# Performance work log

Measured on AMD Instinct MI355X. Metric: run time of the kernel, lower is better.

## Reference

```python
import jax, jax.numpy as jnp
import numpy as np

CODEBOOK_SIZE = 1024
CODEBOOK_DIM = 256
B, H, W = 32, 64, 64


def setup_inputs() -> dict:
    key = jax.random.key(0)
    kx, kc = jax.random.split(key)
    x = jax.random.normal(kx, (B, CODEBOOK_DIM, H, W), dtype=jnp.float32)
    # nn.init.uniform_(weight, -1/K, 1/K)
    bound = 1.0 / CODEBOOK_SIZE
    codebook = jax.random.uniform(kc, (CODEBOOK_SIZE, CODEBOOK_DIM),
                                  minval=-bound, maxval=bound, dtype=jnp.float32)
    return {"x": x, "codebook": codebook}


def reference(x, codebook):
    b, c, h, w = x.shape
    z_e = jnp.transpose(x, (0, 2, 3, 1))            # [b,h,w,c]
    z_flat = z_e.reshape(-1, c)                      # [N,c]
    # squared L2 distances: ||z||^2 + ||e||^2 - 2 z.e
    dists = (jnp.sum(z_flat * z_flat, axis=1, keepdims=True)
             + jnp.sum(codebook * codebook, axis=1)
             - 2.0 * jnp.matmul(z_flat, codebook.T))  # [N,K]
    idx = jnp.argmin(dists, axis=1)                  # [N] int
    z_q = codebook[idx].reshape(b, h, w, c)          # [b,h,w,c]
    # commitment + codebook loss (both detach patterns)
    loss = (jnp.mean((jax.lax.stop_gradient(z_e) - z_q) ** 2)
            + jnp.mean((jax.lax.stop_gradient(z_q) - z_e) ** 2))
    # straight-through estimator
    z_q_st = z_e + jax.lax.stop_gradient(z_q - z_e)
    z_q_out = jnp.transpose(z_q_st, (0, 3, 1, 2))    # [b,c,h,w]
    return z_q_out, idx, loss
```

## Files before the change

kernel.cpp:

```cpp
#include <hip/hip_runtime.h>


typedef __attribute__((ext_vector_type(8))) short short8;
typedef __attribute__((ext_vector_type(4))) float f32x4;
typedef unsigned long long u64;

#define IDX_OFF   33554432u
#define LOSS_OFF  33685504u
#define IMG_BYTE  67108864u
#define CAND_BYTE 68157440u
#define ENRM_BYTE 69206016u

__device__ __forceinline__ unsigned short f2bf(float f) {
  unsigned u = __float_as_uint(f);
  unsigned r = (u + 0x7FFFu + ((u >> 16) & 1u)) >> 16;
  return (unsigned short)r;
}

#define COMB(r) __fadd_rn(__fadd_rn(__fadd_rn(r[0], r[1]), __fadd_rn(r[2], r[3])), \
                          __fadd_rn(__fadd_rn(r[4], r[5]), __fadd_rn(r[6], r[7])))

extern "C" __global__ __launch_bounds__(256) void vq_r10_k0(const float* __restrict__ cb,
                                                            unsigned char* __restrict__ img,
                                                            float* __restrict__ outf) {
  unsigned tid = blockIdx.x * 256u + threadIdx.x;
  unsigned code = tid >> 7, dp = tid & 127u;
  const float* p = cb + (size_t)code * 256u + dp * 2u;
  unsigned u = ((unsigned)f2bf(p[1]) << 16) | (unsigned)f2bf(p[0]);
  unsigned kc = code >> 6, n = (code >> 4) & 3, c16 = code & 15;
  unsigned ks = dp >> 4, g = (dp >> 2) & 3, j = dp & 3;
  unsigned byte = kc * 32768u + (n * 8u + ks) * 1024u + (g * 16u + c16) * 16u + j * 4u;
  *(unsigned*)(img + byte) = u;
  if (tid == 0) outf[LOSS_OFF] = 0.0f;
}

extern "C" __global__ __launch_bounds__(256) void vq_r10_k0b(const float* __restrict__ cb,
                                                             float* __restrict__ enrm) {
#pragma clang fp contract(off)
  int c = blockIdx.x * 256 + threadIdx.x;
  const float* e = cb + (size_t)c * 256u;
  float h[2];
#pragma unroll
  for (int half = 0; half < 2; ++half) {
    float r[8];
#pragma unroll
    for (int j = 0; j < 8; ++j) {
      float v = e[half * 128 + j];
      r[j] = __fmul_rn(v, v);
    }
    for (int i = 8; i < 128; i += 8) {
#pragma unroll
      for (int j = 0; j < 8; ++j) {
        float v = e[half * 128 + i + j];
        r[j] = __fadd_rn(r[j], __fmul_rn(v, v));
      }
    }
    h[half] = COMB(r);
  }
  enrm[c] = __fadd_rn(h[0], h[1]);
}

extern "C" __global__ __launch_bounds__(256, 2) void vq_r10_k1(const float* __restrict__ x,
                                                               const unsigned char* __restrict__ img,
                                                               u64* __restrict__ cand4) {
  __shared__ __attribute__((aligned(16))) char lds[32768];
  const int t = threadIdx.x;
  const int bid = blockIdx.x;
  const int lane = t & 63;
  const int w = t >> 6;
  const int g = lane >> 4, c16 = lane & 15;

  const size_t xbase = (size_t)(bid >> 4) * 1048576u + (size_t)(bid & 15) * 256u;

  short8 a[4][8];
  for (int q = 0; q < 4; ++q) {
#pragma unroll 4
    for (int s = 0; s < 8; ++s) {
      int flat = s * 256 + t;
      int pt4 = flat & 15;
      int dp = flat >> 4;
      const float* px = x + xbase + (size_t)(2 * dp) * 4096u + (unsigned)(q * 64 + pt4 * 4);
      float4 fa = *(const float4*)px;
      float4 fb = *(const float4*)(px + 4096);
      const float* fap = (const float*)&fa;
      const float* fbp = (const float*)&fb;
#pragma unroll
      for (int k = 0; k < 4; ++k) {
        unsigned u = ((unsigned)f2bf(fbp[k]) << 16) | (unsigned)f2bf(fap[k]);
        int r = pt4 * 4 + k;
        *(unsigned*)(lds + r * 512 + ((dp * 4) ^ ((r & 31) << 2))) = u;
      }
    }
    __syncthreads();
    if (w == q) {
#pragma unroll
      for (int m = 0; m < 4; ++m) {
        const int r = m * 16 + c16;
        const int rsw = (r & 31) << 2;
#pragma unroll
        for (int ks = 0; ks < 8; ++ks) {
          union { unsigned q4[4]; short8 s8; } uu;
#pragma unroll
          for (int jj = 0; jj < 4; ++jj)
            uu.q4[jj] = *(const unsigned*)(lds + r * 512 + (((ks * 16 + g * 4 + jj) * 4) ^ rsw));
          a[m][ks] = uu.s8;
        }
      }
    }
    __syncthreads();
  }

  float t1[16], t2[16];
#pragma unroll
  for (int s = 0; s < 16; ++s) { t1[s] = -__builtin_inff(); t2[s] = -__builtin_inff(); }

  const unsigned char* bp = img + (unsigned)(lane * 16);
  for (int kc = 0; kc < 16; ++kc) {
    const unsigned char* bkc = bp + (unsigned)(kc * 32768);
#pragma unroll
    for (int n = 0; n < 4; ++n) {
      short8 bf[8];
#pragma unroll
      for (int ks = 0; ks < 8; ++ks)
        bf[ks] = *(const short8*)(bkc + (unsigned)((n * 8 + ks) * 1024));
      f32x4 acc0 = (f32x4){0.f, 0.f, 0.f, 0.f};
      f32x4 acc1 = (f32x4){0.f, 0.f, 0.f, 0.f};
      f32x4 acc2 = (f32x4){0.f, 0.f, 0.f, 0.f};
      f32x4 acc3 = (f32x4){0.f, 0.f, 0.f, 0.f};
#pragma unroll
      for (int ks = 0; ks < 8; ++ks) {
        acc0 = __builtin_amdgcn_mfma_f32_16x16x32_bf16(a[0][ks], bf[ks], acc0, 0, 0, 0);
        acc1 = __builtin_amdgcn_mfma_f32_16x16x32_bf16(a[1][ks], bf[ks], acc1, 0, 0, 0);
        acc2 = __builtin_amdgcn_mfma_f32_16x16x32_bf16(a[2][ks], bf[ks], acc2, 0, 0, 0);
        acc3 = __builtin_amdgcn_mfma_f32_16x16x32_bf16(a[3][ks], bf[ks], acc3, 0, 0, 0);
      }
      const unsigned code = (unsigned)(kc * 64 + n * 16 + c16);
#define SCRN(v, s) { float kf = __uint_as_float((__float_as_uint(v) & 0xFFFFFC00u) | code); \
                     t2[s] = __builtin_amdgcn_fmed3f(kf, t1[s], t2[s]); \
                     t1[s] = fmaxf(t1[s], kf); }
#pragma unroll
      for (int i = 0; i < 4; ++i) {
        SCRN(acc0[i], i);
        SCRN(acc1[i], 4 + i);
        SCRN(acc2[i], 8 + i);
        SCRN(acc3[i], 12 + i);
      }
#undef SCRN
    }
  }

  __syncthreads();
  float* kk = (float*)lds;
#pragma unroll
  for (int m = 0; m < 4; ++m)
#pragma unroll
    for (int i = 0; i < 4; ++i) {
      int pt = w * 64 + m * 16 + g * 4 + i;
      kk[pt * 32 + c16 * 2] = t1[m * 4 + i];
      kk[pt * 32 + c16 * 2 + 1] = t2[m * 4 + i];
    }
  __syncthreads();

  {
    float f1 = -__builtin_inff(), f2v = f1, f3 = f1, f4 = f1;
#pragma unroll
    for (int j = 0; j < 32; ++j) {
      float v = kk[t * 32 + ((j + t) & 31)];
      float b1 = fminf(f1, v);   f1 = fmaxf(f1, v);
      float b2 = fminf(f2v, b1); f2v = fmaxf(f2v, b1);
      float b3 = fminf(f3, b2);  f3 = fmaxf(f3, b2);
      f4 = fmaxf(f4, b3);
    }
    u64 pk = (u64)(__float_as_uint(f1) & 1023u)
           | ((u64)(__float_as_uint(f2v) & 1023u) << 16)
           | ((u64)(__float_as_uint(f3) & 1023u) << 32)
           | ((u64)(__float_as_uint(f4) & 1023u) << 48);
    cand4[(size_t)bid * 256u + (unsigned)t] = pk;
  }
}

extern "C" __global__ __launch_bounds__(256) void vq_r10_k2(const float* __restrict__ x,
                                                            const float* __restrict__ cb,
                                                            const u64* __restrict__ cand4,
                                                            const float* __restrict__ enrm,
                                                            float* __restrict__ outf) {
#pragma clang fp contract(off)
  __shared__ double dts[4][64];
  __shared__ float s1s[64];
  const int t = threadIdx.x;
  const int pl = t & 63;
  const int c = t >> 6;
  const unsigned p = blockIdx.x * 64u + (unsigned)pl;

  const u64 pk = cand4[p];
  const int code = (int)((pk >> (16 * c)) & 1023u);

  const size_t xoff = ((size_t)(p >> 12)) * 1048576u + (size_t)(p & 4095u);
  const float* e = cb + (size_t)code * 256u;

  double da = 0.0, db = 0.0;
  float hs1[2];
#pragma unroll
  for (int half = 0; half < 2; ++half) {
    float r[8];
#pragma unroll 2
    for (int i = 0; i < 128; i += 8) {
      const int dbase = half * 128 + i;
      float q[8], xv[8];
      *(float4*)(q) = *(const float4*)(e + dbase);
      *(float4*)(q + 4) = *(const float4*)(e + dbase + 4);
#pragma unroll
      for (int j = 0; j < 8; ++j) xv[j] = x[xoff + (size_t)(dbase + j) * 4096u];
#pragma unroll
      for (int j = 0; j < 8; ++j) {
        r[j] = (i == 0) ? __fmul_rn(xv[j], xv[j])
                        : __fadd_rn(r[j], __fmul_rn(xv[j], xv[j]));
        if (j & 1) db = fma((double)xv[j], (double)q[j], db);
        else       da = fma((double)xv[j], (double)q[j], da);
      }
    }
    hs1[half] = COMB(r);
  }
  dts[c][pl] = da + db;
  if (c == 0) s1s[pl] = __fadd_rn(hs1[0], hs1[1]);
  __syncthreads();

  if (t < 64) {
    const float s1v = s1s[pl];
    float bestd = __builtin_inff();
    int besti = 0x7FFFFFFF;
#pragma unroll
    for (int cc = 0; cc < 4; ++cc) {
      const int ccode = (int)((pk >> (16 * cc)) & 1023u);
      float dd = __fsub_rn(__fadd_rn(s1v, enrm[ccode]),
                           __fmul_rn(2.0f, (float)dts[cc][pl]));
      if (dd < bestd || (dd == bestd && ccode < besti)) { bestd = dd; besti = ccode; }
    }
    outf[IDX_OFF + p] = (float)besti;

    float sum = bestd;
#pragma unroll
    for (int off = 32; off > 0; off >>= 1) sum += __shfl_down(sum, off);
    if (pl == 0) atomicAdd(outf + LOSS_OFF, sum);
  }
}

extern "C" __global__ void vq_r10_k4(float* __restrict__ outf) {
  if (threadIdx.x == 0 && blockIdx.x == 0)
    outf[LOSS_OFF] = 2.0f * (outf[LOSS_OFF] / 33554432.0f);
}

extern "C" __global__ __launch_bounds__(256) void vq_r10_k3(const float* __restrict__ cb,
                                                            float* __restrict__ outf) {
  __shared__ float rows[32 * 257];
  const int t = threadIdx.x;
  const unsigned p0 = blockIdx.x * 32u;
  const unsigned b = p0 >> 12, hw0 = p0 & 4095u;
  const float* idxf = outf + IDX_OFF;
  for (int i = 0; i < 32; ++i) {
    int row = ((int)idxf[p0 + (unsigned)i]) & 1023;
    rows[i * 257 + t] = cb[(size_t)row * 256u + (unsigned)t];
  }
  __syncthreads();
  const int j = t & 31, chh = t >> 5;
  float* obase = outf + (size_t)b * 1048576u + hw0 + (unsigned)j;
#pragma unroll
  for (int cc = 0; cc < 32; ++cc) {
    int c = chh * 32 + cc;
    obase[(size_t)c * 4096u] = rows[j * 257 + c];
  }
}

extern "C" void kernel_launch(void* const* d_in, const int* in_sizes, int n_in,
                              void* d_out, int out_size, void* d_ws, size_t ws_size,
                              hipStream_t stream) {
  const float* x = (const float*)d_in[0];
  const float* cb = (const float*)d_in[1];
  float* outf = (float*)d_out;
  unsigned char* img = (unsigned char*)d_out + IMG_BYTE;
  u64* cand4 = (u64*)((unsigned char*)d_out + CAND_BYTE);
  float* enrm = (float*)((unsigned char*)d_out + ENRM_BYTE);
  (void)in_sizes; (void)n_in; (void)out_size; (void)d_ws; (void)ws_size;

  vq_r10_k0<<<512, 256, 0, stream>>>(cb, img, outf);
  vq_r10_k0b<<<4, 256, 0, stream>>>(cb, enrm);
  vq_r10_k1<<<512, 256, 0, stream>>>(x, img, cand4);
  vq_r10_k2<<<2048, 256, 0, stream>>>(x, cb, cand4, enrm, outf);
  vq_r10_k4<<<1, 64, 0, stream>>>(outf);
  vq_r10_k3<<<4096, 256, 0, stream>>>(cb, outf);
}
```

Measured before the change: 205.5 us.

## Double-buffer codebook fragments into LDS via async global_load_lds and vectorize scatter

The distance kernel now streams each wave's codebook B-fragments from global memory into a per-wave double-buffered LDS region with global_load_lds. The next slice is prefetched while the current one feeds the MFMAs, with explicit waitcnt fences. This aims to hide global-load latency that was previously exposed before each group of MFMAs. LDS use doubles to 64 KB, which may limit occupancy. The gather/transpose output kernel also switches from scalar stores to float4 stores for better write coalescing.

```diff
diff --git a/kernel.cpp b/kernel.cpp
--- a/kernel.cpp
+++ b/kernel.cpp
@@ -20,7 +20,7 @@
 #define COMB(r) __fadd_rn(__fadd_rn(__fadd_rn(r[0], r[1]), __fadd_rn(r[2], r[3])), \
                           __fadd_rn(__fadd_rn(r[4], r[5]), __fadd_rn(r[6], r[7])))
 
-extern "C" __global__ __launch_bounds__(256) void vq_r10_k0(const float* __restrict__ cb,
+extern "C" __global__ __launch_bounds__(256) void vq_r11_k0(const float* __restrict__ cb,
                                                             unsigned char* __restrict__ img,
                                                             float* __restrict__ outf) {
   unsigned tid = blockIdx.x * 256u + threadIdx.x;
@@ -34,7 +34,7 @@
   if (tid == 0) outf[LOSS_OFF] = 0.0f;
 }
 
-extern "C" __global__ __launch_bounds__(256) void vq_r10_k0b(const float* __restrict__ cb,
+extern "C" __global__ __launch_bounds__(256) void vq_r11_k0b(const float* __restrict__ cb,
                                                              float* __restrict__ enrm) {
 #pragma clang fp contract(off)
   int c = blockIdx.x * 256 + threadIdx.x;
@@ -60,10 +60,19 @@
   enrm[c] = __fadd_rn(h[0], h[1]);
 }
 
-extern "C" __global__ __launch_bounds__(256, 2) void vq_r10_k1(const float* __restrict__ x,
+__device__ __forceinline__ void issue_frags(const unsigned char* gsrc, char* ldst) {
+#pragma unroll
+  for (int ks = 0; ks < 8; ++ks)
+    __builtin_amdgcn_global_load_lds(
+        (const __attribute__((address_space(1))) unsigned int*)(gsrc + ks * 1024),
+        (__attribute__((address_space(3))) unsigned int*)(ldst + ks * 1024),
+        16, 0, 0);
+}
+
+extern "C" __global__ __launch_bounds__(256, 2) void vq_r11_k1(const float* __restrict__ x,
                                                                const unsigned char* __restrict__ img,
                                                                u64* __restrict__ cand4) {
-  __shared__ __attribute__((aligned(16))) char lds[32768];
+  __shared__ __attribute__((aligned(16))) char lds[65536];
   const int t = threadIdx.x;
   const int bid = blockIdx.x;
   const int lane = t & 63;
@@ -114,39 +123,45 @@
 #pragma unroll
   for (int s = 0; s < 16; ++s) { t1[s] = -__builtin_inff(); t2[s] = -__builtin_inff(); }
 
-  const unsigned char* bp = img + (unsigned)(lane * 16);
-  for (int kc = 0; kc < 16; ++kc) {
-    const unsigned char* bkc = bp + (unsigned)(kc * 32768);
-#pragma unroll
-    for (int n = 0; n < 4; ++n) {
-      short8 bf[8];
-#pragma unroll
-      for (int ks = 0; ks < 8; ++ks)
-        bf[ks] = *(const short8*)(bkc + (unsigned)((n * 8 + ks) * 1024));
-      f32x4 acc0 = (f32x4){0.f, 0.f, 0.f, 0.f};
-      f32x4 acc1 = (f32x4){0.f, 0.f, 0.f, 0.f};
-      f32x4 acc2 = (f32x4){0.f, 0.f, 0.f, 0.f};
-      f32x4 acc3 = (f32x4){0.f, 0.f, 0.f, 0.f};
-#pragma unroll
-      for (int ks = 0; ks < 8; ++ks) {
-        acc0 = __builtin_amdgcn_mfma_f32_16x16x32_bf16(a[0][ks], bf[ks], acc0, 0, 0, 0);
-        acc1 = __builtin_amdgcn_mfma_f32_16x16x32_bf16(a[1][ks], bf[ks], acc1, 0, 0, 0);
-        acc2 = __builtin_amdgcn_mfma_f32_16x16x32_bf16(a[2][ks], bf[ks], acc2, 0, 0, 0);
-        acc3 = __builtin_amdgcn_mfma_f32_16x16x32_bf16(a[3][ks], bf[ks], acc3, 0, 0, 0);
-      }
-      const unsigned code = (unsigned)(kc * 64 + n * 16 + c16);
-#define SCRN(v, s) { float kf = __uint_as_float((__float_as_uint(v) & 0xFFFFFC00u) | code); \
-                     t2[s] = __builtin_amdgcn_fmed3f(kf, t1[s], t2[s]); \
-                     t1[s] = fmaxf(t1[s], kf); }
-#pragma unroll
-      for (int i = 0; i < 4; ++i) {
-        SCRN(acc0[i], i);
-        SCRN(acc1[i], 4 + i);
-        SCRN(acc2[i], 8 + i);
-        SCRN(acc3[i], 12 + i);
-      }
+  char* ldsW = lds + w * 16384;
+  const unsigned char* gW = img + (unsigned)(lane * 16);
+
+  issue_frags(gW, ldsW);
+
+  for (int s = 0; s < 64; ++s) {
+    char* cur = ldsW + (s & 1) * 8192;
+    asm volatile("s_waitcnt lgkmcnt(0)" ::: "memory");
+    if (s < 63) {
+      issue_frags(gW + (unsigned)((s + 1) * 8192), ldsW + ((s + 1) & 1) * 8192);
+      asm volatile("s_waitcnt vmcnt(8)" ::: "memory");
+    } else {
+      asm volatile("s_waitcnt vmcnt(0)" ::: "memory");
+    }
+
+    f32x4 acc0 = (f32x4){0.f, 0.f, 0.f, 0.f};
+    f32x4 acc1 = (f32x4){0.f, 0.f, 0.f, 0.f};
+    f32x4 acc2 = (f32x4){0.f, 0.f, 0.f, 0.f};
+    f32x4 acc3 = (f32x4){0.f, 0.f, 0.f, 0.f};
+#pragma unroll
+    for (int ks = 0; ks < 8; ++ks) {
+      short8 b = *(const short8*)(cur + ks * 1024 + lane * 16);
+      acc0 = __builtin_amdgcn_mfma_f32_16x16x32_bf16(a[0][ks], b, acc0, 0, 0, 0);
+      acc1 = __builtin_amdgcn_mfma_f32_16x16x32_bf16(a[1][ks], b, acc1, 0, 0, 0);
+      acc2 = __builtin_amdgcn_mfma_f32_16x16x32_bf16(a[2][ks], b, acc2, 0, 0, 0);
+      acc3 = __builtin_amdgcn_mfma_f32_16x16x32_bf16(a[3][ks], b, acc3, 0, 0, 0);
+    }
+    const unsigned code = (unsigned)(s * 16 + c16);
+#define SCRN(v, sl) { float kf = __uint_as_float((__float_as_uint(v) & 0xFFFFFC00u) | code); \
+                      t2[sl] = __builtin_amdgcn_fmed3f(kf, t1[sl], t2[sl]); \
+                      t1[sl] = fmaxf(t1[sl], kf); }
+#pragma unroll
+    for (int i = 0; i < 4; ++i) {
+      SCRN(acc0[i], i);
+      SCRN(acc1[i], 4 + i);
+      SCRN(acc2[i], 8 + i);
+      SCRN(acc3[i], 12 + i);
+    }
 #undef SCRN
-    }
   }
 
   __syncthreads();
@@ -179,7 +194,7 @@
   }
 }
 
-extern "C" __global__ __launch_bounds__(256) void vq_r10_k2(const float* __restrict__ x,
+extern "C" __global__ __launch_bounds__(256) void vq_r11_k2(const float* __restrict__ x,
                                                             const float* __restrict__ cb,
                                                             const u64* __restrict__ cand4,
                                                             const float* __restrict__ enrm,
@@ -245,12 +260,12 @@
   }
 }
 
-extern "C" __global__ void vq_r10_k4(float* __restrict__ outf) {
+extern "C" __global__ void vq_r11_k4(float* __restrict__ outf) {
   if (threadIdx.x == 0 && blockIdx.x == 0)
     outf[LOSS_OFF] = 2.0f * (outf[LOSS_OFF] / 33554432.0f);
 }
 
-extern "C" __global__ __launch_bounds__(256) void vq_r10_k3(const float* __restrict__ cb,
+extern "C" __global__ __launch_bounds__(256) void vq_r11_k3(const float* __restrict__ cb,
                                                             float* __restrict__ outf) {
   __shared__ float rows[32 * 257];
   const int t = threadIdx.x;
@@ -262,12 +277,17 @@
     rows[i * 257 + t] = cb[(size_t)row * 256u + (unsigned)t];
   }
   __syncthreads();
-  const int j = t & 31, chh = t >> 5;
-  float* obase = outf + (size_t)b * 1048576u + hw0 + (unsigned)j;
-#pragma unroll
-  for (int cc = 0; cc < 32; ++cc) {
-    int c = chh * 32 + cc;
-    obase[(size_t)c * 4096u] = rows[j * 257 + c];
+  const int q = t & 7, cgrp = t >> 3;
+  float* obase = outf + (size_t)b * 1048576u + hw0 + (unsigned)(q * 4);
+#pragma unroll
+  for (int cc = 0; cc < 8; ++cc) {
+    int c = cgrp * 8 + cc;
+    float4 v;
+    v.x = rows[(q * 4 + 0) * 257 + c];
+    v.y = rows[(q * 4 + 1) * 257 + c];
+    v.z = rows[(q * 4 + 2) * 257 + c];
+    v.w = rows[(q * 4 + 3) * 257 + c];
+    *(float4*)(obase + (size_t)c * 4096u) = v;
   }
 }
 
@@ -282,10 +302,10 @@
   float* enrm = (float*)((unsigned char*)d_out + ENRM_BYTE);
   (void)in_sizes; (void)n_in; (void)out_size; (void)d_ws; (void)ws_size;
 
-  vq_r10_k0<<<512, 256, 0, stream>>>(cb, img, outf);
-  vq_r10_k0b<<<4, 256, 0, stream>>>(cb, enrm);
-  vq_r10_k1<<<512, 256, 0, stream>>>(x, img, cand4);
-  vq_r10_k2<<<2048, 256, 0, stream>>>(x, cb, cand4, enrm, outf);
-  vq_r10_k4<<<1, 64, 0, stream>>>(outf);
-  vq_r10_k3<<<4096, 256, 0, stream>>>(cb, outf);
-}
+  vq_r11_k0<<<512, 256, 0, stream>>>(cb, img, outf);
+  vq_r11_k0b<<<4, 256, 0, stream>>>(cb, enrm);
+  vq_r11_k1<<<512, 256, 0, stream>>>(x, img, cand4);
+  vq_r11_k2<<<2048, 256, 0, stream>>>(x, cb, cand4, enrm, outf);
+  vq_r11_k4<<<1, 64, 0, stream>>>(outf);
+  vq_r11_k3<<<4096, 256, 0, stream>>>(cb, outf);
+}
```

After: 214.2 us. 4.2% more time.
